# Kernel optimization log

Hardware: AMD Instinct MI355X
Metric: run time of the kernel (lower is better)

The kernel has to match this reference:

```python
import jax, jax.numpy as jnp
import numpy as np

T, B, I, H = 1024, 64, 3, 2048


def setup_inputs() -> dict:
    key = jax.random.key(0)
    ks = jax.random.split(key, 6)
    lim = 1.0 / np.sqrt(H).astype(np.float32)  # eqx GRUCell init range
    return {
        "inp": jax.random.normal(ks[0], (T, B, I), jnp.float32),
        "init_hidden": jax.random.normal(ks[1], (B, H), jnp.float32),
        "weight_ih": jax.random.uniform(ks[2], (3 * H, I), jnp.float32, -lim, lim),
        "weight_hh": jax.random.uniform(ks[3], (3 * H, H), jnp.float32, -lim, lim),
        "bias": jax.random.uniform(ks[4], (3 * H,), jnp.float32, -lim, lim),
        "bias_n": jax.random.uniform(ks[5], (H,), jnp.float32, -lim, lim),
    }


def reference(inp, init_hidden, weight_ih, weight_hh, bias, bias_n):
    # Input projections for all timesteps at once: [T, B, 3H]
    igates_all = jnp.einsum("tbi,gi->tbg", inp, weight_ih) + bias

    def step(h, ig):
        hg = h @ weight_hh.T  # [B, 3H]
        ig_r, ig_z, ig_n = jnp.split(ig, 3, axis=-1)
        hg_r, hg_z, hg_n = jnp.split(hg, 3, axis=-1)
        reset = jax.nn.sigmoid(ig_r + hg_r)
        upd = jax.nn.sigmoid(ig_z + hg_z)
        new = jnp.tanh(ig_n + reset * (hg_n + bias_n))
        h_new = new + upd * (h - new)  # eqx GRUCell: new + inp_gate*(hidden-new)
        return h_new, h_new[:, 0]      # out = first hidden unit per step

    _, out = jax.lax.scan(step, init_hidden, igates_all)
    return out  # [T, B]
```

## Files before the change

kernel.cpp:

```cpp
#include <hip/hip_runtime.h>

typedef __attribute__((ext_vector_type(8))) short bf16x8;
typedef __attribute__((ext_vector_type(4))) float f32x4;
typedef __attribute__((ext_vector_type(4))) int i32x4;

#define Tn 1024
#define Bn 64
#define Hn 2048
#define NBLK 256
#define NTHR 512

#define GRP(ring, leaf, g) (((((ring) << 7) | ((leaf) << 3) | (g))) * 32)

#define SPIN_LIMIT (1u << 25)

__device__ __forceinline__ unsigned short f2b(float x) {
    unsigned u = __float_as_uint(x);
    return (unsigned short)((u + 0x7fffu + ((u >> 16) & 1u)) >> 16);
}
__device__ __forceinline__ float sigm(float x) {
    return __builtin_amdgcn_rcpf(1.0f + __expf(-x));
}
__device__ __forceinline__ float tanh_f(float x) {
    float e = __expf(2.0f * x);
    return 1.0f - 2.0f * __builtin_amdgcn_rcpf(1.0f + e);
}

__device__ __forceinline__ void store_short_wt(unsigned short* p, unsigned v) {
    asm volatile("global_store_short %0, %1, off sc0 sc1" :: "v"(p), "v"(v) : "memory");
}
__device__ __forceinline__ void store_dword_wt(float* p, float v) {
    asm volatile("global_store_dword %0, %1, off sc0 sc1" :: "v"(p), "v"(__float_as_uint(v)) : "memory");
}
__device__ __forceinline__ void store_u64_wt(unsigned long long* p, unsigned long long v) {
    asm volatile("global_store_dwordx2 %0, %1, off sc0 sc1" :: "v"(p), "v"(v) : "memory");
}
__device__ __forceinline__ unsigned poll_read(unsigned* p) {
    unsigned old;
    asm volatile("global_atomic_add %0, %1, %2, off sc0 sc1\n\ts_waitcnt vmcnt(0)"
                 : "=v"(old) : "v"(p), "v"(0u) : "memory");
    return old;
}

__device__ __forceinline__ long hfrag_off(int b, int k) {
    return ((long)(((k >> 5) * 4 + (b >> 4)) * 64) + ((k >> 3) & 3) * 16 + (b & 15)) * 8 + (k & 7);
}

__global__ void prep_kernel(const float* __restrict__ init_h,
                            unsigned short* __restrict__ h0,
                            unsigned* __restrict__ ctrl) {
    const int i = blockIdx.x * 256 + threadIdx.x;
    const int b  = i >> 9;
    const int k4 = (i & 511) << 2;
    float4 v = *reinterpret_cast<const float4*>(init_h + (long)b * Hn + k4);
    unsigned long long q = (unsigned long long)f2b(v.x)
                         | ((unsigned long long)f2b(v.y) << 16)
                         | ((unsigned long long)f2b(v.z) << 32)
                         | ((unsigned long long)f2b(v.w) << 48);
    store_u64_wt((unsigned long long*)(h0 + hfrag_off(b, k4)), q);
    if (i < 8192)
        asm volatile("global_store_dword %0, %1, off sc0 sc1"
                     :: "v"(ctrl + i), "v"(0u) : "memory");
}

__global__ void __launch_bounds__(NTHR, 2) gru_kernel(
    const float* __restrict__ inp,
    const float* __restrict__ init_h,
    const float* __restrict__ w_ih,
    const float* __restrict__ w_hh,
    const float* __restrict__ bias,
    const float* __restrict__ bias_n,
    unsigned short* __restrict__ h0,
    unsigned short* __restrict__ h1,
    unsigned* __restrict__ ctrl,
    float* __restrict__ out)
{
    __shared__ f32x4 red[4][2][3][64];

    const int tid  = threadIdx.x;
    const int lane = tid & 63;
    const int w    = tid >> 6;
    const int quad = lane >> 4;
    const int n16  = lane & 15;
    const int R    = blockIdx.x & 1;
    const int c    = blockIdx.x >> 1;
    const int jg   = c * 16 + n16;
    const int ks   = w * 256;
    const int bbase = 32 * R;

    bf16x8 Bf[3][8];
    #pragma unroll
    for (int nt = 0; nt < 3; ++nt) {
        const long row = (long)(nt * Hn + jg);
        #pragma unroll
        for (int k = 0; k < 8; ++k) {
            const float* p = w_hh + row * Hn + ks + k * 32 + quad * 8;
            bf16x8 b;
            #pragma unroll
            for (int j = 0; j < 8; ++j) b[j] = (short)f2b(p[j]);
            Bf[nt][k] = b;
        }
    }

    float wr0 = w_ih[jg*3+0], wr1 = w_ih[jg*3+1], wr2 = w_ih[jg*3+2];
    float wz0 = w_ih[(Hn+jg)*3+0], wz1 = w_ih[(Hn+jg)*3+1], wz2 = w_ih[(Hn+jg)*3+2];
    float wn0 = w_ih[(2*Hn+jg)*3+0], wn1 = w_ih[(2*Hn+jg)*3+1], wn2 = w_ih[(2*Hn+jg)*3+2];
    float br_ = bias[jg], bz_ = bias[Hn+jg], bn2_ = bias[2*Hn+jg];
    float bnn_ = bias_n[jg];

    float hst[4];
    if (w < 2) {
        #pragma unroll
        for (int r = 0; r < 4; ++r)
            hst[r] = init_h[(long)(bbase + 16 * w + quad * 4 + r) * Hn + jg];
    }

    const int kkE = c >> 1;
    const int qE  = (c & 1) * 2 + (n16 >> 3);
    const int eE  = n16 & 7;

    const int leafC = c >> 3;
    const int grp   = c >> 4;

    for (int t = 0; t < Tn; ++t) {
        const unsigned short* hcur = (t & 1) ? h1 : h0;
        unsigned short* hnext      = (t & 1) ? h0 : h1;

        float xv[4][3];
        if (w < 2) {
            #pragma unroll
            for (int r = 0; r < 4; ++r) {
                const float* xp = inp + ((long)t * Bn + bbase + 16 * w + quad * 4 + r) * 3;
                xv[r][0] = xp[0]; xv[r][1] = xp[1]; xv[r][2] = xp[2];
            }
        }

        f32x4 acc[2][3];
        #pragma unroll
        for (int m = 0; m < 2; ++m)
            #pragma unroll
            for (int nt = 0; nt < 3; ++nt)
                acc[m][nt] = f32x4{0.f, 0.f, 0.f, 0.f};

        if (lane == 0 && t) {
            const unsigned tgt = (unsigned)(t << 4);
            unsigned spins = 0;
            while (poll_read(&ctrl[GRP(R, leafC, w)]) < tgt) {
                __builtin_amdgcn_s_sleep(1);
                if (++spins > SPIN_LIMIT) break;
            }
        }

        const unsigned short* pa = hcur + ((long)(32 * w + 2 * R) * 64 + lane) * 8;

        i32x4 hb[16];
        #pragma unroll
        for (int kki = 0; kki < 8; ++kki) {
            #pragma unroll
            for (int m = 0; m < 2; ++m) {
                asm volatile("global_load_dwordx4 %0, %1, off sc0 sc1"
                             : "=v"(hb[kki * 2 + m])
                             : "v"(pa + (long)(kki * 4 + m) * 512) : "memory");
            }
        }
        asm volatile("s_waitcnt vmcnt(8)"
                     : "+v"(hb[0]), "+v"(hb[1]), "+v"(hb[2]), "+v"(hb[3]),
                       "+v"(hb[4]), "+v"(hb[5]), "+v"(hb[6]), "+v"(hb[7])
                     :: "memory");
        __builtin_amdgcn_s_setprio(1);
        #pragma unroll
        for (int kki = 0; kki < 4; ++kki) {
            #pragma unroll
            for (int m = 0; m < 2; ++m) {
                union { i32x4 q; bf16x8 v; } u;
                u.q = hb[kki * 2 + m];
                bf16x8 a = u.v;
                acc[m][0] = __builtin_amdgcn_mfma_f32_16x16x32_bf16(a, Bf[0][kki], acc[m][0], 0, 0, 0);
                acc[m][1] = __builtin_amdgcn_mfma_f32_16x16x32_bf16(a, Bf[1][kki], acc[m][1], 0, 0, 0);
                acc[m][2] = __builtin_amdgcn_mfma_f32_16x16x32_bf16(a, Bf[2][kki], acc[m][2], 0, 0, 0);
            }
        }
        __builtin_amdgcn_s_setprio(0);
        asm volatile("s_waitcnt vmcnt(0)"
                     : "+v"(hb[8]), "+v"(hb[9]), "+v"(hb[10]), "+v"(hb[11]),
                       "+v"(hb[12]), "+v"(hb[13]), "+v"(hb[14]), "+v"(hb[15])
                     :: "memory");
        __builtin_amdgcn_s_setprio(1);
        #pragma unroll
        for (int kki = 4; kki < 8; ++kki) {
            #pragma unroll
            for (int m = 0; m < 2; ++m) {
                union { i32x4 q; bf16x8 v; } u;
                u.q = hb[kki * 2 + m];
                bf16x8 a = u.v;
                acc[m][0] = __builtin_amdgcn_mfma_f32_16x16x32_bf16(a, Bf[0][kki], acc[m][0], 0, 0, 0);
                acc[m][1] = __builtin_amdgcn_mfma_f32_16x16x32_bf16(a, Bf[1][kki], acc[m][1], 0, 0, 0);
                acc[m][2] = __builtin_amdgcn_mfma_f32_16x16x32_bf16(a, Bf[2][kki], acc[m][2], 0, 0, 0);
            }
        }
        __builtin_amdgcn_s_setprio(0);

        if (w >= 4) {
            #pragma unroll
            for (int m = 0; m < 2; ++m)
                #pragma unroll
                for (int nt = 0; nt < 3; ++nt)
                    red[w - 4][m][nt][lane] = acc[m][nt];
        }
        __syncthreads();
        if (w < 4) {
            #pragma unroll
            for (int m = 0; m < 2; ++m)
                #pragma unroll
                for (int nt = 0; nt < 3; ++nt)
                    acc[m][nt] += red[w][m][nt][lane];
        }
        __syncthreads();
        if (w < 4) {
            #pragma unroll
            for (int m = 0; m < 2; ++m)
                #pragma unroll
                for (int nt = 0; nt < 3; ++nt)
                    red[w][m][nt][lane] = acc[m][nt];
        }
        __syncthreads();

        if (w < 2) {
            f32x4 s0 = red[0][w][0][lane], s1 = red[0][w][1][lane], s2 = red[0][w][2][lane];
            #pragma unroll
            for (int src = 1; src < 4; ++src) {
                s0 += red[src][w][0][lane];
                s1 += red[src][w][1][lane];
                s2 += red[src][w][2][lane];
            }
            #pragma unroll
            for (int r = 0; r < 4; ++r) {
                const int b = bbase + 16 * w + quad * 4 + r;
                float pr = br_ + wr0*xv[r][0] + wr1*xv[r][1] + wr2*xv[r][2] + s0[r];
                float pz = bz_ + wz0*xv[r][0] + wz1*xv[r][1] + wz2*xv[r][2] + s1[r];
                float rr = sigm(pr);
                float zz = sigm(pz);
                float pn = bn2_ + wn0*xv[r][0] + wn1*xv[r][1] + wn2*xv[r][2] + rr * (s2[r] + bnn_);
                float nn = tanh_f(pn);
                float hv = nn + zz * (hst[r] - nn);
                hst[r] = hv;
                store_short_wt(hnext + ((long)((kkE * 4 + 2 * R + w) * 64) + qE * 16 + quad * 4 + r) * 8 + eE,
                               (unsigned)f2b(hv));
                if (c == 0 && n16 == 0)
                    store_dword_wt(out + t * Bn + b, hv);
            }
        }

        asm volatile("s_waitcnt vmcnt(0)" ::: "memory");
        __syncthreads();
        if (tid < 16)
            __hip_atomic_fetch_add(&ctrl[GRP(R, tid, grp)], 1u,
                                   __ATOMIC_RELAXED, __HIP_MEMORY_SCOPE_SYSTEM);
    }
}

extern "C" void kernel_launch(void* const* d_in, const int* in_sizes, int n_in,
                              void* d_out, int out_size, void* d_ws, size_t ws_size,
                              hipStream_t stream) {
    const float* inp    = (const float*)d_in[0];
    const float* init_h = (const float*)d_in[1];
    const float* w_ih   = (const float*)d_in[2];
    const float* w_hh   = (const float*)d_in[3];
    const float* bias   = (const float*)d_in[4];
    const float* bias_n = (const float*)d_in[5];
    float* out = (float*)d_out;

    unsigned short* h0 = (unsigned short*)d_ws;
    unsigned short* h1 = h0 + 131072L;
    unsigned* ctrl     = (unsigned*)(h1 + 131072L);

    prep_kernel<<<128, 256, 0, stream>>>(init_h, h0, ctrl);
    gru_kernel<<<NBLK, NTHR, 0, stream>>>(inp, init_h, w_ih, w_hh, bias, bias_n,
                                          h0, h1, ctrl, out);
}
```

Before: 4.115 ms.

## Use single-barrier 8-way LDS reduction and finer-grained load waits in GRU step

Measured after the change: 3.836 ms. -6.8%, faster.

```diff
diff --git a/kernel.cpp b/kernel.cpp
--- a/kernel.cpp
+++ b/kernel.cpp
@@ -75,7 +75,7 @@
     unsigned* __restrict__ ctrl,
     float* __restrict__ out)
 {
-    __shared__ f32x4 red[4][2][3][64];
+    __shared__ f32x4 red[8][2][3][64];
 
     const int tid  = threadIdx.x;
     const int lane = tid & 63;
@@ -163,13 +163,46 @@
                              : "v"(pa + (long)(kki * 4 + m) * 512) : "memory");
             }
         }
+        asm volatile("s_waitcnt vmcnt(12)"
+                     : "+v"(hb[0]), "+v"(hb[1]), "+v"(hb[2]), "+v"(hb[3])
+                     :: "memory");
+        __builtin_amdgcn_s_setprio(1);
+        #pragma unroll
+        for (int kki = 0; kki < 2; ++kki) {
+            #pragma unroll
+            for (int m = 0; m < 2; ++m) {
+                union { i32x4 q; bf16x8 v; } u;
+                u.q = hb[kki * 2 + m];
+                bf16x8 a = u.v;
+                acc[m][0] = __builtin_amdgcn_mfma_f32_16x16x32_bf16(a, Bf[0][kki], acc[m][0], 0, 0, 0);
+                acc[m][1] = __builtin_amdgcn_mfma_f32_16x16x32_bf16(a, Bf[1][kki], acc[m][1], 0, 0, 0);
+                acc[m][2] = __builtin_amdgcn_mfma_f32_16x16x32_bf16(a, Bf[2][kki], acc[m][2], 0, 0, 0);
+            }
+        }
+        __builtin_amdgcn_s_setprio(0);
         asm volatile("s_waitcnt vmcnt(8)"
-                     : "+v"(hb[0]), "+v"(hb[1]), "+v"(hb[2]), "+v"(hb[3]),
-                       "+v"(hb[4]), "+v"(hb[5]), "+v"(hb[6]), "+v"(hb[7])
-                     :: "memory");
-        __builtin_amdgcn_s_setprio(1);
-        #pragma unroll
-        for (int kki = 0; kki < 4; ++kki) {
+                     : "+v"(hb[4]), "+v"(hb[5]), "+v"(hb[6]), "+v"(hb[7])
+                     :: "memory");
+        __builtin_amdgcn_s_setprio(1);
+        #pragma unroll
+        for (int kki = 2; kki < 4; ++kki) {
+            #pragma unroll
+            for (int m = 0; m < 2; ++m) {
+                union { i32x4 q; bf16x8 v; } u;
+                u.q = hb[kki * 2 + m];
+                bf16x8 a = u.v;
+                acc[m][0] = __builtin_amdgcn_mfma_f32_16x16x32_bf16(a, Bf[0][kki], acc[m][0], 0, 0, 0);
+                acc[m][1] = __builtin_amdgcn_mfma_f32_16x16x32_bf16(a, Bf[1][kki], acc[m][1], 0, 0, 0);
+                acc[m][2] = __builtin_amdgcn_mfma_f32_16x16x32_bf16(a, Bf[2][kki], acc[m][2], 0, 0, 0);
+            }
+        }
+        __builtin_amdgcn_s_setprio(0);
+        asm volatile("s_waitcnt vmcnt(4)"
+                     : "+v"(hb[8]), "+v"(hb[9]), "+v"(hb[10]), "+v"(hb[11])
+                     :: "memory");
+        __builtin_amdgcn_s_setprio(1);
+        #pragma unroll
+        for (int kki = 4; kki < 6; ++kki) {
             #pragma unroll
             for (int m = 0; m < 2; ++m) {
                 union { i32x4 q; bf16x8 v; } u;
@@ -182,53 +215,34 @@
         }
         __builtin_amdgcn_s_setprio(0);
         asm volatile("s_waitcnt vmcnt(0)"
-                     : "+v"(hb[8]), "+v"(hb[9]), "+v"(hb[10]), "+v"(hb[11]),
-                       "+v"(hb[12]), "+v"(hb[13]), "+v"(hb[14]), "+v"(hb[15])
-                     :: "memory");
-        __builtin_amdgcn_s_setprio(1);
-        #pragma unroll
-        for (int kki = 4; kki < 8; ++kki) {
-            #pragma unroll
-            for (int m = 0; m < 2; ++m) {
-                union { i32x4 q; bf16x8 v; } u;
-                u.q = hb[kki * 2 + m];
-                bf16x8 a = u.v;
-                acc[m][0] = __builtin_amdgcn_mfma_f32_16x16x32_bf16(a, Bf[0][kki], acc[m][0], 0, 0, 0);
-                acc[m][1] = __builtin_amdgcn_mfma_f32_16x16x32_bf16(a, Bf[1][kki], acc[m][1], 0, 0, 0);
-                acc[m][2] = __builtin_amdgcn_mfma_f32_16x16x32_bf16(a, Bf[2][kki], acc[m][2], 0, 0, 0);
-            }
-        }
-        __builtin_amdgcn_s_setprio(0);
-
-        if (w >= 4) {
-            #pragma unroll
-            for (int m = 0; m < 2; ++m)
-                #pragma unroll
-                for (int nt = 0; nt < 3; ++nt)
-                    red[w - 4][m][nt][lane] = acc[m][nt];
-        }
-        __syncthreads();
-        if (w < 4) {
-            #pragma unroll
-            for (int m = 0; m < 2; ++m)
-                #pragma unroll
-                for (int nt = 0; nt < 3; ++nt)
-                    acc[m][nt] += red[w][m][nt][lane];
-        }
-        __syncthreads();
-        if (w < 4) {
-            #pragma unroll
-            for (int m = 0; m < 2; ++m)
-                #pragma unroll
-                for (int nt = 0; nt < 3; ++nt)
-                    red[w][m][nt][lane] = acc[m][nt];
-        }
+                     : "+v"(hb[12]), "+v"(hb[13]), "+v"(hb[14]), "+v"(hb[15])
+                     :: "memory");
+        __builtin_amdgcn_s_setprio(1);
+        #pragma unroll
+        for (int kki = 6; kki < 8; ++kki) {
+            #pragma unroll
+            for (int m = 0; m < 2; ++m) {
+                union { i32x4 q; bf16x8 v; } u;
+                u.q = hb[kki * 2 + m];
+                bf16x8 a = u.v;
+                acc[m][0] = __builtin_amdgcn_mfma_f32_16x16x32_bf16(a, Bf[0][kki], acc[m][0], 0, 0, 0);
+                acc[m][1] = __builtin_amdgcn_mfma_f32_16x16x32_bf16(a, Bf[1][kki], acc[m][1], 0, 0, 0);
+                acc[m][2] = __builtin_amdgcn_mfma_f32_16x16x32_bf16(a, Bf[2][kki], acc[m][2], 0, 0, 0);
+            }
+        }
+        __builtin_amdgcn_s_setprio(0);
+
+        #pragma unroll
+        for (int m = 0; m < 2; ++m)
+            #pragma unroll
+            for (int nt = 0; nt < 3; ++nt)
+                red[w][m][nt][lane] = acc[m][nt];
         __syncthreads();
 
         if (w < 2) {
             f32x4 s0 = red[0][w][0][lane], s1 = red[0][w][1][lane], s2 = red[0][w][2][lane];
             #pragma unroll
-            for (int src = 1; src < 4; ++src) {
+            for (int src = 1; src < 8; ++src) {
                 s0 += red[src][w][0][lane];
                 s1 += red[src][w][1][lane];
                 s2 += red[src][w][2][lane];
```
